# Optimization experiments

Hardware: AMD Instinct MI355X
Metric: run time of the kernel (lower is better)

Reference implementation:

```python
import math
import jax, jax.numpy as jnp
import numpy as np

D_MODEL = 1024
N_HEAD = 16
D_HEAD = 64
Q_LEN = 2048
MEM_LEN = 2048
K_LEN = MEM_LEN + Q_LEN
B = 1
LN_EPS = 1e-5


def setup_inputs() -> dict:
    key = jax.random.key(0)
    ks = jax.random.split(key, 8)
    hidden = jax.random.normal(ks[0], (B, Q_LEN, D_MODEL), dtype=jnp.float32)
    position_embedding = jax.random.normal(ks[1], (K_LEN, D_MODEL), dtype=jnp.float32)
    u = jax.random.normal(ks[2], (N_HEAD, D_HEAD), dtype=jnp.float32) * 0.02
    v = jax.random.normal(ks[3], (N_HEAD, D_HEAD), dtype=jnp.float32) * 0.02
    memory = jax.random.normal(ks[4], (B, MEM_LEN, D_MODEL), dtype=jnp.float32)
    # TXL causal mask: query i may attend to key j iff j <= i + MEM_LEN
    i = jnp.arange(Q_LEN)[:, None]
    j = jnp.arange(K_LEN)[None, :]
    mask = (j > (i + MEM_LEN))[None, None]  # (1,1,Q,K) bool, True = masked
    # weights (torch Linear has no bias here); stored as (in, out)
    s = 1.0 / math.sqrt(D_MODEL)
    W_qkv = jax.random.normal(ks[5], (D_MODEL, 3 * N_HEAD * D_HEAD), dtype=jnp.float32) * s
    W_pe = jax.random.normal(ks[6], (D_MODEL, N_HEAD * D_HEAD), dtype=jnp.float32) * s
    W_out = jax.random.normal(ks[7], (N_HEAD * D_HEAD, D_MODEL), dtype=jnp.float32) * (1.0 / math.sqrt(N_HEAD * D_HEAD))
    return {"hidden": hidden, "position_embedding": position_embedding, "u": u,
            "v": v, "mask": mask, "memory": memory,
            "W_qkv": W_qkv, "W_pe": W_pe, "W_out": W_out}


def _layer_norm(x):
    # elementwise_affine=False LayerNorm over last dim
    mu = jnp.mean(x, axis=-1, keepdims=True)
    var = jnp.var(x, axis=-1, keepdims=True)
    return (x - mu) / jnp.sqrt(var + LN_EPS)


def reference(hidden, position_embedding, u, v, mask, memory, W_qkv, W_pe, W_out):
    batch, q_len, _ = hidden.shape
    k_len = position_embedding.shape[0]
    scale = 1.0 / math.sqrt(D_HEAD)

    mh = jnp.concatenate([memory, hidden], axis=1)          # (B, k_len, d_model)
    qkv = mh @ W_qkv                                        # post-norm: no LN on input
    Q, K, V = jnp.split(qkv, 3, axis=-1)
    Q = Q[:, -q_len:, :]
    pe = position_embedding @ W_pe                          # (k_len, H*D)

    Q = Q.reshape(batch, q_len, N_HEAD, D_HEAD)
    K = K.reshape(batch, k_len, N_HEAD, D_HEAD)
    V = V.reshape(batch, k_len, N_HEAD, D_HEAD)
    pe = pe.reshape(batch, k_len, N_HEAD, D_HEAD)

    AC = jnp.einsum('bqhd,bkhd->bhqk', Q + u, K)
    BD = jnp.einsum('bqhd,bkhd->bhqk', Q + v, pe)
    # NOTE: the original module calls relative_shift(BD) but DISCARDS the
    # result, so BD is used unshifted. We faithfully reproduce that.
    score = (AC + BD) * scale
    score = jnp.where(mask, -jnp.inf, score)
    prob = jax.nn.softmax(score, axis=-1)                   # (B,H,Q,K)
    av = jnp.einsum('bhqk,bkhd->bqhd', prob, V)
    av = av.reshape(batch, q_len, N_HEAD * D_HEAD)
    attn_out = av @ W_out
    return _layer_norm(hidden + attn_out)                   # post-norm residual
```

## Files before the change

kernel.cpp:

```cpp
#include <hip/hip_runtime.h>

typedef __attribute__((ext_vector_type(4))) float f32x4;
typedef __attribute__((ext_vector_type(16))) float f32x16;
typedef __attribute__((ext_vector_type(8))) short bf16x8;
typedef __attribute__((ext_vector_type(4))) unsigned short u16x4;
typedef unsigned short u16;

#define DM 1024
#define NHEAD 16
#define DHEAD 64
#define QLEN 2048
#define MLEN 2048
#define KLEN 4096

__device__ __forceinline__ float bf2f(u16 u) {
    unsigned i = ((unsigned)u) << 16; float f; __builtin_memcpy(&f, &i, 4); return f;
}
__device__ __forceinline__ u16 f2bf(float f) {
    unsigned i; __builtin_memcpy(&i, &f, 4);
    unsigned r = i + 0x7fffu + ((i >> 16) & 1u);
    return (u16)(r >> 16);
}
__device__ __forceinline__ unsigned cvtpk_bf16(float lo, float hi) {
    unsigned r;
    asm("v_cvt_pk_bf16_f32 %0, %1, %2" : "=v"(r) : "v"(lo), "v"(hi));
    return r;
}
__device__ __forceinline__ void gl2lds16(const void* g, void* l) {
    __builtin_amdgcn_global_load_lds((const __attribute__((address_space(1))) void*)g,
                                     (__attribute__((address_space(3))) void*)l, 16, 0, 0);
}

__global__ __launch_bounds__(256) void prep(
    const float* __restrict__ memory, const float* __restrict__ hidden,
    const float* __restrict__ pos, const float* __restrict__ Wqkv,
    const float* __restrict__ Wpe, const float* __restrict__ Wout,
    u16* __restrict__ MH, u16* __restrict__ PEA,
    u16* __restrict__ WQKVT, u16* __restrict__ WPET, u16* __restrict__ WOUTT)
{
    __shared__ float ls[64][65];
    const int b = blockIdx.x, t = threadIdx.x;
    if (b < 8192) {
        size_t e = ((size_t)b * 256 + t) * 4;
        const size_t HALF = (size_t)KLEN * DM;
        f32x4 v; u16* dst;
        if (e < HALF) {
            size_t row = e >> 10, col = e & 1023;
            const float* src = (row < MLEN) ? (memory + row * DM) : (hidden + (row - MLEN) * DM);
            v = *(const f32x4*)(src + col);
            dst = MH + e;
        } else {
            size_t e2 = e - HALF;
            v = *(const f32x4*)(pos + e2);
            dst = PEA + e2;
        }
        u16x4 o;
        #pragma unroll
        for (int c = 0; c < 4; ++c) o[c] = f2bf(v[c]);
        *(u16x4*)dst = o;
        return;
    }
    int tb = b - 8192;
    const float* src; u16* dst; int N, bx, by;
    if (tb < 768)       { src = Wqkv; dst = WQKVT; N = 3 * DM; bx = tb % 48; by = tb / 48; }
    else if (tb < 1024) { int i = tb - 768;  src = Wpe;  dst = WPET;  N = DM; bx = i & 15; by = i >> 4; }
    else                { int i = tb - 1024; src = Wout; dst = WOUTT; N = DM; bx = i & 15; by = i >> 4; }
    const int n0 = bx * 64, k0 = by * 64;
    const int c = t & 63, rg = t >> 6;
    #pragma unroll
    for (int p = 0; p < 16; ++p) {
        int r = p * 4 + rg;
        ls[r][c] = src[(size_t)(k0 + r) * N + n0 + c];
    }
    __syncthreads();
    #pragma unroll
    for (int p = 0; p < 16; ++p) {
        int r = p * 4 + rg;
        dst[(size_t)(n0 + r) * DM + k0 + c] = f2bf(ls[c][r]);
    }
}

__global__ __launch_bounds__(256, 3) void gemm_qkvpe(
    const u16* __restrict__ MH, const u16* __restrict__ PEA,
    const u16* __restrict__ WQKVT, const u16* __restrict__ WPET,
    const float* __restrict__ u, const float* __restrict__ vv,
    u16* __restrict__ QHAT, u16* __restrict__ KHAT, u16* __restrict__ VB)
{
    __shared__ u16 lsA[128 * 64];
    __shared__ u16 lsB[128 * 64];
    const int b = blockIdx.x;
    int row0, col0, region; const u16 *A, *B;
    if (b < 512)      { row0 = (b >> 4) * 128; col0 = 1024 + (b & 15) * 128; A = MH; B = WQKVT;
                        region = (col0 < 2048) ? 1 : 2; }
    else if (b < 640) { int i = b - 512; row0 = 2048 + (i >> 3) * 128; col0 = (i & 7) * 128;
                        A = MH; B = WQKVT; region = 0; }
    else              { int i = b - 640; row0 = (i >> 3) * 128; col0 = (i & 7) * 128;
                        A = PEA; B = WPET; region = 3; }
    const int tid = threadIdx.x, wave = tid >> 6, lane = tid & 63;
    const int blk = lane >> 4, ln = lane & 15;
    const int wr = (wave >> 1) << 6, wc = (wave & 1) << 6;
    const int rstage = lane >> 3;
    const int cstage = (lane & 7) * 8;

    f32x4 acc[4][4];
    #pragma unroll
    for (int i = 0; i < 4; ++i)
        #pragma unroll
        for (int j = 0; j < 4; ++j) acc[i][j] = f32x4{0.f, 0.f, 0.f, 0.f};

    for (int k0 = 0; k0 < DM; k0 += 64) {
        #pragma unroll
        for (int t = 0; t < 4; ++t) {
            int chunk = wave * 4 + t;
            int r = chunk * 8 + rstage;
            gl2lds16(A + (size_t)(row0 + r) * DM + k0 + cstage, lsA + chunk * 512);
            gl2lds16(B + (size_t)(col0 + r) * DM + k0 + cstage, lsB + chunk * 512);
        }
        __syncthreads();
        #pragma unroll
        for (int kk = 0; kk < 2; ++kk) {
            bf16x8 af[4], bfr[4];
            #pragma unroll
            for (int i = 0; i < 4; ++i)
                af[i] = *(const bf16x8*)(lsA + (wr + i * 16 + ln) * 64 + kk * 32 + blk * 8);
            #pragma unroll
            for (int j = 0; j < 4; ++j)
                bfr[j] = *(const bf16x8*)(lsB + (wc + j * 16 + ln) * 64 + kk * 32 + blk * 8);
            #pragma unroll
            for (int i = 0; i < 4; ++i)
                #pragma unroll
                for (int j = 0; j < 4; ++j)
                    acc[i][j] = __builtin_amdgcn_mfma_f32_16x16x32_bf16(af[i], bfr[j], acc[i][j], 0, 0, 0);
        }
        __syncthreads();
    }
    #pragma unroll
    for (int i = 0; i < 4; ++i)
        #pragma unroll
        for (int j = 0; j < 4; ++j)
            #pragma unroll
            for (int r = 0; r < 4; ++r) {
                int row = row0 + wr + i * 16 + blk * 4 + r;
                int col = col0 + wc + j * 16 + ln;
                float val = acc[i][j][r];
                if (region == 0) {
                    int q = row - MLEN, h = col >> 6;
                    size_t base = ((size_t)h * QLEN + q) * 128 + (col & 63);
                    QHAT[base]      = f2bf((val + u[col]) * 0.125f);
                    QHAT[base + 64] = f2bf((val + vv[col]) * 0.125f);
                } else if (region == 1) {
                    int c = col - 1024, h = c >> 6;
                    KHAT[((size_t)h * KLEN + row) * 128 + (c & 63)] = f2bf(val);
                } else if (region == 2) {
                    VB[(size_t)row * DM + (col - 2048)] = f2bf(val);
                } else {
                    int h = col >> 6;
                    KHAT[((size_t)h * KLEN + row) * 128 + 64 + (col & 63)] = f2bf(val);
                }
            }
}

__global__ __launch_bounds__(256) void pack_vt(const u16* __restrict__ VB, u16* __restrict__ VT)
{
    __shared__ float ls[64][65];
    const int kt = blockIdx.x, h = blockIdx.y;
    const int t = threadIdx.x, c = t & 63, rg = t >> 6;
    #pragma unroll
    for (int p = 0; p < 16; ++p) {
        int r = p * 4 + rg;
        ls[r][c] = bf2f(VB[(size_t)(kt * 64 + r) * DM + h * 64 + c]);
    }
    __syncthreads();
    #pragma unroll
    for (int p = 0; p < 16; ++p) {
        int d = p * 4 + rg;
        VT[((size_t)h * DHEAD + d) * KLEN + kt * 64 + c] = f2bf(ls[c][d]);
    }
}

__global__ __launch_bounds__(256, 4) void attn_fused(
    const u16* __restrict__ QHAT, const u16* __restrict__ KHAT,
    const u16* __restrict__ VT, u16* __restrict__ OPb, float* __restrict__ ML)
{
    __shared__ __align__(16) u16 smem[18432];
    const int b = blockIdx.x;
    const int h  = ((b & 7) << 1) | ((b >> 3) & 1);
    const int ks = b >> 8;
    const int qb = (((b >> 4) & 15) + 4 * ks) & 15;
    const int tid = threadIdx.x;
    const int wave = tid >> 6, lane = tid & 63;
    const int l31 = lane & 31, hi = lane >> 5;
    const int qrow0 = qb * 128 + wave * 32;
    u16* pb = smem + 13312 + wave * 1280;
    const int px = (l31 >> 3) & 3;

    const u16* khp = KHAT + (size_t)h * KLEN * 128;
    const u16* vhp = VT + (size_t)h * DHEAD * KLEN;

    const int nt = qb + 17;
    const int kbase = ks * nt * 32;
    const int vd = tid >> 2, vc = tid & 3;
    const int vslot = vc ^ ((vd >> 3) & 3);

    auto stage_load = [&](int buf, int kt) -> bf16x8 {
        const int k0 = kbase + kt * 32;
        u16* Kb = smem + buf * 4096;
        #pragma unroll
        for (int i = 0; i < 2; ++i) {
            int c = i * 256 + tid;
            int row = c >> 4, cgl = c & 15;
            int cs = cgl ^ (row & 15);
            gl2lds16(khp + ((size_t)(k0 + row) << 7) + cs * 8,
                     Kb + (size_t)(i * 256 + (tid & ~63)) * 8);
        }
        return *(const bf16x8*)(vhp + (size_t)vd * KLEN + k0 + vc * 8);
    };
    auto stage_write = [&](int buf, bf16x8 vr) {
        *(bf16x8*)(smem + 8192 + buf * 2560 + vd * 40 + vslot * 8) = vr;
    };

    bf16x8 qf[8];
    {
        const u16* qbase = QHAT + ((size_t)h * QLEN + qrow0 + l31) * 128 + hi * 8;
        #pragma unroll
        for (int kd = 0; kd < 8; ++kd) qf[kd] = *(const bf16x8*)(qbase + kd * 16);
    }

    f32x16 oacc[2];
    #pragma unroll
    for (int dg = 0; dg < 2; ++dg)
        #pragma unroll
        for (int r = 0; r < 16; ++r) oacc[dg][r] = 0.f;
    float mi = -1e30f, li = 0.f;

    const int qlim = qrow0 + 31 + MLEN;
    const int qsel = qrow0 + l31 + MLEN;

    bf16x8 vreg = stage_load(0, 0);
    asm volatile("s_waitcnt vmcnt(0)" ::: "memory");
    stage_write(0, vreg);
    __syncthreads();

    int cur = 0;
    for (int kt = 0; kt < nt; ++kt) {
        const int k0 = kbase + kt * 32;
        const bool pre = (kt + 1 < nt);
        if (pre) vreg = stage_load(cur ^ 1, kt + 1);

        if (k0 <= qlim) {
            f32x16 sacc;
            #pragma unroll
            for (int r = 0; r < 16; ++r) sacc[r] = 0.f;
            const u16* kb = smem + cur * 4096;
            const int rx = l31 & 15;
            #pragma unroll
            for (int kd = 0; kd < 8; ++kd) {
                int cd = (kd * 2 + hi) ^ rx;
                bf16x8 kf = *(const bf16x8*)(kb + l31 * 128 + cd * 8);
                sacc = __builtin_amdgcn_mfma_f32_32x32x16_bf16(kf, qf[kd], sacc, 0, 0, 0);
            }
            if (k0 + 31 > qrow0 + MLEN) {
                const int keyb = k0 + 4 * hi;
                #pragma unroll
                for (int r = 0; r < 16; ++r) {
                    int key = keyb + (r & 3) + 8 * (r >> 2);
                    if (key > qsel) sacc[r] = -1e30f;
                }
            }
            float mt;
            {
                f32x4 m4;
                #pragma unroll
                for (int r = 0; r < 4; ++r)
                    m4[r] = fmaxf(fmaxf(sacc[r], sacc[4 + r]), fmaxf(sacc[8 + r], sacc[12 + r]));
                mt = fmaxf(fmaxf(m4[0], m4[1]), fmaxf(m4[2], m4[3]));
            }
            mt = fmaxf(mt, __shfl_xor(mt, 32, 64));
            if (!__all(mt <= mi)) {
                float mn = fmaxf(mi, mt);
                float corr = __expf(mi - mn);
                mi = mn;
                li *= corr;
                #pragma unroll
                for (int dg = 0; dg < 2; ++dg)
                    #pragma unroll
                    for (int r = 0; r < 16; ++r) oacc[dg][r] *= corr;
            }
            #pragma unroll
            for (int r = 0; r < 16; ++r) sacc[r] = __expf(sacc[r] - mi);
            float rs;
            {
                f32x4 s4;
                #pragma unroll
                for (int r = 0; r < 4; ++r)
                    s4[r] = (sacc[r] + sacc[4 + r]) + (sacc[8 + r] + sacc[12 + r]);
                rs = (s4[0] + s4[1]) + (s4[2] + s4[3]);
            }
            li += rs + __shfl_xor(rs, 32, 64);
            {
                unsigned* pd = (unsigned*)(pb + (size_t)l31 * 40);
                #pragma unroll
                for (int b2 = 0; b2 < 4; ++b2)
                    #pragma unroll
                    for (int c = 0; c < 2; ++c)
                        pd[(b2 ^ px) * 4 + 2 * hi + c] =
                            cvtpk_bf16(sacc[4 * b2 + 2 * c], sacc[4 * b2 + 2 * c + 1]);
            }
            #pragma unroll
            for (int kkl = 0; kkl < 2; ++kkl) {
                bf16x8 pf = *(const bf16x8*)(pb + (size_t)l31 * 40 + ((kkl * 2 + hi) ^ px) * 8);
                #pragma unroll
                for (int dg = 0; dg < 2; ++dg) {
                    int vrow = dg * 32 + l31;
                    int cd = (kkl * 2 + hi) ^ ((l31 >> 3) & 3);
                    bf16x8 vf = *(const bf16x8*)(smem + 8192 + cur * 2560 + vrow * 40 + cd * 8);
                    oacc[dg] = __builtin_amdgcn_mfma_f32_32x32x16_bf16(vf, pf, oacc[dg], 0, 0, 0);
                }
            }
        }
        asm volatile("s_waitcnt vmcnt(0)" ::: "memory");
        if (pre) stage_write(cur ^ 1, vreg);
        __syncthreads();
        cur ^= 1;
    }

    const int q = qrow0 + l31;
    unsigned* op32 = (unsigned*)(OPb + (((size_t)ks * QLEN + q) * NHEAD + h) * 64);
    #pragma unroll
    for (int dg = 0; dg < 2; ++dg) {
        union { f32x16 v; float f[16]; } oo;
        oo.v = oacc[dg];
        #pragma unroll
        for (int b2 = 0; b2 < 4; ++b2)
            #pragma unroll
            for (int c = 0; c < 2; ++c)
                op32[(dg * 32 + 8 * b2 + 4 * hi) / 2 + c] =
                    cvtpk_bf16(oo.f[4 * b2 + 2 * c], oo.f[4 * b2 + 2 * c + 1]);
    }
    if (!hi) {
        float* ml = ML + (((size_t)ks * QLEN + q) * NHEAD + h) * 2;
        ml[0] = mi; ml[1] = li;
    }
}

__global__ __launch_bounds__(256) void attn_combine(
    const u16* __restrict__ OPb, const float* __restrict__ ML, u16* __restrict__ AVB)
{
    int idx = blockIdx.x * 256 + threadIdx.x;
    int d8 = (idx & 7) * 8;
    int h  = (idx >> 3) & 15;
    int q  = idx >> 7;
    float m[4], l[4], mf = -1e30f;
    #pragma unroll
    for (int ks = 0; ks < 4; ++ks) {
        const float* ml = ML + (((size_t)ks * QLEN + q) * NHEAD + h) * 2;
        m[ks] = ml[0]; l[ks] = ml[1];
        mf = fmaxf(mf, m[ks]);
    }
    float lsum = 0.f;
    float a[4];
    #pragma unroll
    for (int ks = 0; ks < 4; ++ks) {
        a[ks] = __expf(m[ks] - mf);
        lsum += a[ks] * l[ks];
    }
    float inv = 1.f / lsum;
    float acc[8];
    #pragma unroll
    for (int j = 0; j < 8; ++j) acc[j] = 0.f;
    #pragma unroll
    for (int ks = 0; ks < 4; ++ks) {
        float w = a[ks] * inv;
        const u16* src = OPb + (((size_t)ks * QLEN + q) * NHEAD + h) * 64 + d8;
        u16x4 x0 = *(const u16x4*)(src);
        u16x4 x1 = *(const u16x4*)(src + 4);
        #pragma unroll
        for (int j = 0; j < 4; ++j) { acc[j] += w * bf2f(x0[j]); acc[4 + j] += w * bf2f(x1[j]); }
    }
    unsigned* A32 = (unsigned*)AVB;
    size_t base = ((size_t)q * DM + h * 64 + d8) >> 1;
    #pragma unroll
    for (int j = 0; j < 4; ++j)
        A32[base + j] = cvtpk_bf16(acc[2 * j], acc[2 * j + 1]);
}

__global__ __launch_bounds__(256, 3) void gemm_out(
    const u16* __restrict__ A, const u16* __restrict__ Bt, float* __restrict__ RES)
{
    __shared__ u16 lsA[128 * 64];
    __shared__ u16 lsB[128 * 64];
    const int b = blockIdx.x;
    const int tile = b >> 1, kh = b & 1;
    const int row0 = (tile >> 3) * 128, col0 = (tile & 7) * 128;
    const int tid = threadIdx.x, wave = tid >> 6, lane = tid & 63;
    const int blk = lane >> 4, ln = lane & 15;
    const int wr = (wave >> 1) << 6, wc = (wave & 1) << 6;
    const int rstage = lane >> 3;
    const int cstage = (lane & 7) * 8;

    f32x4 acc[4][4];
    #pragma unroll
    for (int i = 0; i < 4; ++i)
        #pragma unroll
        for (int j = 0; j < 4; ++j) acc[i][j] = f32x4{0.f, 0.f, 0.f, 0.f};

    for (int k0 = kh * 512; k0 < kh * 512 + 512; k0 += 64) {
        #pragma unroll
        for (int t = 0; t < 4; ++t) {
            int chunk = wave * 4 + t;
            int r = chunk * 8 + rstage;
            gl2lds16(A  + (size_t)(row0 + r) * DM + k0 + cstage, lsA + chunk * 512);
            gl2lds16(Bt + (size_t)(col0 + r) * DM + k0 + cstage, lsB + chunk * 512);
        }
        __syncthreads();
        #pragma unroll
        for (int kk = 0; kk < 2; ++kk) {
            bf16x8 af[4], bfr[4];
            #pragma unroll
            for (int i = 0; i < 4; ++i)
                af[i] = *(const bf16x8*)(lsA + (wr + i * 16 + ln) * 64 + kk * 32 + blk * 8);
            #pragma unroll
            for (int j = 0; j < 4; ++j)
                bfr[j] = *(const bf16x8*)(lsB + (wc + j * 16 + ln) * 64 + kk * 32 + blk * 8);
            #pragma unroll
            for (int i = 0; i < 4; ++i)
                #pragma unroll
                for (int j = 0; j < 4; ++j)
                    acc[i][j] = __builtin_amdgcn_mfma_f32_16x16x32_bf16(af[i], bfr[j], acc[i][j], 0, 0, 0);
        }
        __syncthreads();
    }
    float* C = RES + (size_t)kh * QLEN * DM;
    #pragma unroll
    for (int i = 0; i < 4; ++i)
        #pragma unroll
        for (int j = 0; j < 4; ++j)
            #pragma unroll
            for (int r = 0; r < 4; ++r) {
                int row = row0 + wr + i * 16 + blk * 4 + r;
                int col = col0 + wc + j * 16 + ln;
                C[(size_t)row * DM + col] = acc[i][j][r];
            }
}

__global__ __launch_bounds__(256) void ln_kernel(
    const float* __restrict__ hidden, const float* __restrict__ RES, float* __restrict__ out)
{
    const int row = blockIdx.x, t = threadIdx.x;
    const int wave = t >> 6, lane = t & 63;
    __shared__ float ws[8];
    f32x4 a = ((const f32x4*)(hidden + (size_t)row * DM))[t];
    f32x4 r0 = ((const f32x4*)(RES + (size_t)row * DM))[t];
    f32x4 r1 = ((const f32x4*)(RES + (size_t)(QLEN + row) * DM))[t];
    f32x4 v;
    #pragma unroll
    for (int c = 0; c < 4; ++c) v[c] = a[c] + r0[c] + r1[c];
    float s = v[0] + v[1] + v[2] + v[3];
    float s2 = v[0] * v[0] + v[1] * v[1] + v[2] * v[2] + v[3] * v[3];
    #pragma unroll
    for (int off = 1; off < 64; off <<= 1) {
        s += __shfl_xor(s, off, 64);
        s2 += __shfl_xor(s2, off, 64);
    }
    if (lane == 0) { ws[wave] = s; ws[4 + wave] = s2; }
    __syncthreads();
    float ts = ws[0] + ws[1] + ws[2] + ws[3];
    float ts2 = ws[4] + ws[5] + ws[6] + ws[7];
    float mu = ts * (1.f / DM);
    float var = ts2 * (1.f / DM) - mu * mu;
    float rsq = rsqrtf(var + 1e-5f);
    f32x4 o;
    #pragma unroll
    for (int c = 0; c < 4; ++c) o[c] = (v[c] - mu) * rsq;
    ((f32x4*)(out + (size_t)row * DM))[t] = o;
}

extern "C" void kernel_launch(void* const* d_in, const int* in_sizes, int n_in,
                              void* d_out, int out_size, void* d_ws, size_t ws_size,
                              hipStream_t stream)
{
    const float* hidden = (const float*)d_in[0];
    const float* pos    = (const float*)d_in[1];
    const float* u      = (const float*)d_in[2];
    const float* vv     = (const float*)d_in[3];
    const float* memory = (const float*)d_in[5];
    const float* Wqkv   = (const float*)d_in[6];
    const float* Wpe    = (const float*)d_in[7];
    const float* Wout   = (const float*)d_in[8];
    float* out = (float*)d_out;

    char* w = (char*)d_ws;
    auto alloc = [&](size_t bytes) {
        void* p = (void*)w;
        w += (bytes + 255) & ~(size_t)255;
        return p;
    };
    u16* MH    = (u16*)alloc((size_t)KLEN * DM * 2);
    u16* PEA   = (u16*)alloc((size_t)KLEN * DM * 2);
    u16* WQKVT = (u16*)alloc((size_t)3 * DM * DM * 2);
    u16* WPET  = (u16*)alloc((size_t)DM * DM * 2);
    u16* VB    = (u16*)alloc((size_t)KLEN * DM * 2);
    u16* QHAT  = (u16*)alloc((size_t)NHEAD * QLEN * 128 * 2);
    u16* KHAT  = (u16*)alloc((size_t)NHEAD * KLEN * 128 * 2);
    u16* VTb   = (u16*)alloc((size_t)NHEAD * DHEAD * KLEN * 2);
    u16* AVB   = (u16*)alloc((size_t)QLEN * DM * 2);
    float* RES = (float*)alloc((size_t)2 * QLEN * DM * 4);
    u16* WOUTT = (u16*)alloc((size_t)DM * DM * 2);
    u16* OPb   = (u16*)d_ws;
    float* ML  = (float*)((char*)d_ws + (size_t)4 * QLEN * NHEAD * 64 * 2);

    prep<<<8192 + 1280, 256, 0, stream>>>(memory, hidden, pos, Wqkv, Wpe, Wout,
                                          MH, PEA, WQKVT, WPET, WOUTT);
    gemm_qkvpe<<<896, 256, 0, stream>>>(MH, PEA, WQKVT, WPET, u, vv, QHAT, KHAT, VB);
    pack_vt<<<dim3(KLEN / 64, NHEAD), 256, 0, stream>>>(VB, VTb);
    attn_fused<<<dim3(1024), 256, 0, stream>>>(QHAT, KHAT, VTb, OPb, ML);
    attn_combine<<<dim3(QLEN * NHEAD * 8 / 256), 256, 0, stream>>>(OPb, ML, AVB);
    gemm_out<<<256, 256, 0, stream>>>(AVB, WOUTT, RES);
    ln_kernel<<<QLEN, 256, 0, stream>>>(hidden, RES, out);
}
```

Before: 163.4 us.

## Software-pipeline QK^T one tile ahead of softmax-PV and use exp2 with log2e-folded scale

The attention loop is restructured so the QK^T MFMA for the next key tile runs before the softmax and PV of the current tile. K and V loads are issued two tiles ahead using an unrolled A/B double buffer. The Q scale now folds in log2(e), so the exponentials become native exp2 instructions, and the combine kernel uses exp2 as well. Launch bounds drop from 4 to 3 waves per SIMD to give room for the extra live score registers, which may lower occupancy.

```diff
diff --git a/kernel.cpp b/kernel.cpp
--- a/kernel.cpp
+++ b/kernel.cpp
@@ -12,6 +12,7 @@
 #define QLEN 2048
 #define MLEN 2048
 #define KLEN 4096
+#define QSCALE 0.18033688011112042f
 
 __device__ __forceinline__ float bf2f(u16 u) {
     unsigned i = ((unsigned)u) << 16; float f; __builtin_memcpy(&f, &i, 4); return f;
@@ -20,6 +21,13 @@
     unsigned i; __builtin_memcpy(&i, &f, 4);
     unsigned r = i + 0x7fffu + ((i >> 16) & 1u);
     return (u16)(r >> 16);
+}
+__device__ __forceinline__ float exp2_fast(float x) {
+#if __has_builtin(__builtin_amdgcn_exp2f)
+    return __builtin_amdgcn_exp2f(x);
+#else
+    return exp2f(x);
+#endif
 }
 __device__ __forceinline__ unsigned cvtpk_bf16(float lo, float hi) {
     unsigned r;
@@ -146,8 +154,8 @@
                 if (region == 0) {
                     int q = row - MLEN, h = col >> 6;
                     size_t base = ((size_t)h * QLEN + q) * 128 + (col & 63);
-                    QHAT[base]      = f2bf((val + u[col]) * 0.125f);
-                    QHAT[base + 64] = f2bf((val + vv[col]) * 0.125f);
+                    QHAT[base]      = f2bf((val + u[col]) * QSCALE);
+                    QHAT[base + 64] = f2bf((val + vv[col]) * QSCALE);
                 } else if (region == 1) {
                     int c = col - 1024, h = c >> 6;
                     KHAT[((size_t)h * KLEN + row) * 128 + (c & 63)] = f2bf(val);
@@ -178,7 +186,7 @@
     }
 }
 
-__global__ __launch_bounds__(256, 4) void attn_fused(
+__global__ __launch_bounds__(256, 3) void attn_fused(
     const u16* __restrict__ QHAT, const u16* __restrict__ KHAT,
     const u16* __restrict__ VT, u16* __restrict__ OPb, float* __restrict__ ML)
 {
@@ -202,7 +210,10 @@
     const int vd = tid >> 2, vc = tid & 3;
     const int vslot = vc ^ ((vd >> 3) & 3);
 
-    auto stage_load = [&](int buf, int kt) -> bf16x8 {
+    const int qlim = qrow0 + 31 + MLEN;
+    const int qsel = qrow0 + l31 + MLEN;
+
+    auto stageK = [&](int buf, int kt) {
         const int k0 = kbase + kt * 32;
         u16* Kb = smem + buf * 4096;
         #pragma unroll
@@ -213,9 +224,11 @@
             gl2lds16(khp + ((size_t)(k0 + row) << 7) + cs * 8,
                      Kb + (size_t)(i * 256 + (tid & ~63)) * 8);
         }
-        return *(const bf16x8*)(vhp + (size_t)vd * KLEN + k0 + vc * 8);
     };
-    auto stage_write = [&](int buf, bf16x8 vr) {
+    auto loadV = [&](int kt) -> bf16x8 {
+        return *(const bf16x8*)(vhp + (size_t)vd * KLEN + kbase + kt * 32 + vc * 8);
+    };
+    auto writeV = [&](int buf, bf16x8 vr) {
         *(bf16x8*)(smem + 8192 + buf * 2560 + vd * 40 + vslot * 8) = vr;
     };
 
@@ -233,95 +246,112 @@
         for (int r = 0; r < 16; ++r) oacc[dg][r] = 0.f;
     float mi = -1e30f, li = 0.f;
 
-    const int qlim = qrow0 + 31 + MLEN;
-    const int qsel = qrow0 + l31 + MLEN;
-
-    bf16x8 vreg = stage_load(0, 0);
+    auto qk = [&](int buf) -> f32x16 {
+        f32x16 s;
+        #pragma unroll
+        for (int r = 0; r < 16; ++r) s[r] = 0.f;
+        const u16* kb = smem + buf * 4096;
+        const int rx = l31 & 15;
+        #pragma unroll
+        for (int kd = 0; kd < 8; ++kd) {
+            int cd = (kd * 2 + hi) ^ rx;
+            bf16x8 kf = *(const bf16x8*)(kb + l31 * 128 + cd * 8);
+            s = __builtin_amdgcn_mfma_f32_32x32x16_bf16(kf, qf[kd], s, 0, 0, 0);
+        }
+        return s;
+    };
+
+    auto smpv = [&](f32x16& sacc, int buf, int k0) {
+        if (k0 + 31 > qrow0 + MLEN) {
+            const int keyb = k0 + 4 * hi;
+            #pragma unroll
+            for (int r = 0; r < 16; ++r) {
+                int key = keyb + (r & 3) + 8 * (r >> 2);
+                if (key > qsel) sacc[r] = -1e30f;
+            }
+        }
+        float mt;
+        {
+            f32x4 m4;
+            #pragma unroll
+            for (int r = 0; r < 4; ++r)
+                m4[r] = fmaxf(fmaxf(sacc[r], sacc[4 + r]), fmaxf(sacc[8 + r], sacc[12 + r]));
+            mt = fmaxf(fmaxf(m4[0], m4[1]), fmaxf(m4[2], m4[3]));
+        }
+        mt = fmaxf(mt, __shfl_xor(mt, 32, 64));
+        if (!__all(mt <= mi)) {
+            float mn = fmaxf(mi, mt);
+            float corr = exp2_fast(mi - mn);
+            mi = mn;
+            li *= corr;
+            #pragma unroll
+            for (int dg = 0; dg < 2; ++dg)
+                #pragma unroll
+                for (int r = 0; r < 16; ++r) oacc[dg][r] *= corr;
+        }
+        #pragma unroll
+        for (int r = 0; r < 16; ++r) sacc[r] = exp2_fast(sacc[r] - mi);
+        float rs;
+        {
+            f32x4 s4;
+            #pragma unroll
+            for (int r = 0; r < 4; ++r)
+                s4[r] = (sacc[r] + sacc[4 + r]) + (sacc[8 + r] + sacc[12 + r]);
+            rs = (s4[0] + s4[1]) + (s4[2] + s4[3]);
+        }
+        li += rs + __shfl_xor(rs, 32, 64);
+        {
+            unsigned* pd = (unsigned*)(pb + (size_t)l31 * 40);
+            #pragma unroll
+            for (int b2 = 0; b2 < 4; ++b2)
+                #pragma unroll
+                for (int c = 0; c < 2; ++c)
+                    pd[(b2 ^ px) * 4 + 2 * hi + c] =
+                        cvtpk_bf16(sacc[4 * b2 + 2 * c], sacc[4 * b2 + 2 * c + 1]);
+        }
+        #pragma unroll
+        for (int kkl = 0; kkl < 2; ++kkl) {
+            bf16x8 pf = *(const bf16x8*)(pb + (size_t)l31 * 40 + ((kkl * 2 + hi) ^ px) * 8);
+            #pragma unroll
+            for (int dg = 0; dg < 2; ++dg) {
+                int vrow = dg * 32 + l31;
+                int cd = (kkl * 2 + hi) ^ ((l31 >> 3) & 3);
+                bf16x8 vf = *(const bf16x8*)(smem + 8192 + buf * 2560 + vrow * 40 + cd * 8);
+                oacc[dg] = __builtin_amdgcn_mfma_f32_32x32x16_bf16(vf, pf, oacc[dg], 0, 0, 0);
+            }
+        }
+    };
+
+    stageK(0, 0);
+    bf16x8 vrA = loadV(0);
+    bf16x8 vrB = vrA;
+    if (nt > 1) { stageK(1, 1); vrB = loadV(1); }
     asm volatile("s_waitcnt vmcnt(0)" ::: "memory");
-    stage_write(0, vreg);
     __syncthreads();
-
-    int cur = 0;
-    for (int kt = 0; kt < nt; ++kt) {
-        const int k0 = kbase + kt * 32;
-        const bool pre = (kt + 1 < nt);
-        if (pre) vreg = stage_load(cur ^ 1, kt + 1);
-
-        if (k0 <= qlim) {
-            f32x16 sacc;
-            #pragma unroll
-            for (int r = 0; r < 16; ++r) sacc[r] = 0.f;
-            const u16* kb = smem + cur * 4096;
-            const int rx = l31 & 15;
-            #pragma unroll
-            for (int kd = 0; kd < 8; ++kd) {
-                int cd = (kd * 2 + hi) ^ rx;
-                bf16x8 kf = *(const bf16x8*)(kb + l31 * 128 + cd * 8);
-                sacc = __builtin_amdgcn_mfma_f32_32x32x16_bf16(kf, qf[kd], sacc, 0, 0, 0);
-            }
-            if (k0 + 31 > qrow0 + MLEN) {
-                const int keyb = k0 + 4 * hi;
-                #pragma unroll
-                for (int r = 0; r < 16; ++r) {
-                    int key = keyb + (r & 3) + 8 * (r >> 2);
-                    if (key > qsel) sacc[r] = -1e30f;
-                }
-            }
-            float mt;
-            {
-                f32x4 m4;
-                #pragma unroll
-                for (int r = 0; r < 4; ++r)
-                    m4[r] = fmaxf(fmaxf(sacc[r], sacc[4 + r]), fmaxf(sacc[8 + r], sacc[12 + r]));
-                mt = fmaxf(fmaxf(m4[0], m4[1]), fmaxf(m4[2], m4[3]));
-            }
-            mt = fmaxf(mt, __shfl_xor(mt, 32, 64));
-            if (!__all(mt <= mi)) {
-                float mn = fmaxf(mi, mt);
-                float corr = __expf(mi - mn);
-                mi = mn;
-                li *= corr;
-                #pragma unroll
-                for (int dg = 0; dg < 2; ++dg)
-                    #pragma unroll
-                    for (int r = 0; r < 16; ++r) oacc[dg][r] *= corr;
-            }
-            #pragma unroll
-            for (int r = 0; r < 16; ++r) sacc[r] = __expf(sacc[r] - mi);
-            float rs;
-            {
-                f32x4 s4;
-                #pragma unroll
-                for (int r = 0; r < 4; ++r)
-                    s4[r] = (sacc[r] + sacc[4 + r]) + (sacc[8 + r] + sacc[12 + r]);
-                rs = (s4[0] + s4[1]) + (s4[2] + s4[3]);
-            }
-            li += rs + __shfl_xor(rs, 32, 64);
-            {
-                unsigned* pd = (unsigned*)(pb + (size_t)l31 * 40);
-                #pragma unroll
-                for (int b2 = 0; b2 < 4; ++b2)
-                    #pragma unroll
-                    for (int c = 0; c < 2; ++c)
-                        pd[(b2 ^ px) * 4 + 2 * hi + c] =
-                            cvtpk_bf16(sacc[4 * b2 + 2 * c], sacc[4 * b2 + 2 * c + 1]);
-            }
-            #pragma unroll
-            for (int kkl = 0; kkl < 2; ++kkl) {
-                bf16x8 pf = *(const bf16x8*)(pb + (size_t)l31 * 40 + ((kkl * 2 + hi) ^ px) * 8);
-                #pragma unroll
-                for (int dg = 0; dg < 2; ++dg) {
-                    int vrow = dg * 32 + l31;
-                    int cd = (kkl * 2 + hi) ^ ((l31 >> 3) & 3);
-                    bf16x8 vf = *(const bf16x8*)(smem + 8192 + cur * 2560 + vrow * 40 + cd * 8);
-                    oacc[dg] = __builtin_amdgcn_mfma_f32_32x32x16_bf16(vf, pf, oacc[dg], 0, 0, 0);
-                }
-            }
-        }
-        asm volatile("s_waitcnt vmcnt(0)" ::: "memory");
-        if (pre) stage_write(cur ^ 1, vreg);
-        __syncthreads();
-        cur ^= 1;
+    f32x16 sA = qk(0);
+    writeV(0, vrA);
+    __syncthreads();
+    f32x16 sB;
+
+    for (int t = 0; t < nt; t += 2) {
+        {
+            const int k0 = kbase + t * 32;
+            if (t + 2 < nt) { stageK(0, t + 2); vrA = loadV(t + 2); }
+            if (t + 1 < nt) sB = qk(1);
+            if (k0 <= qlim) smpv(sA, 0, k0);
+            if (t + 1 < nt) writeV(1, vrB);
+            asm volatile("s_waitcnt vmcnt(0)" ::: "memory");
+            __syncthreads();
+        }
+        if (t + 1 < nt) {
+            const int k0 = kbase + (t + 1) * 32;
+            if (t + 3 < nt) { stageK(1, t + 3); vrB = loadV(t + 3); }
+            if (t + 2 < nt) sA = qk(0);
+            if (k0 <= qlim) smpv(sB, 1, k0);
+            if (t + 2 < nt) writeV(0, vrA);
+            asm volatile("s_waitcnt vmcnt(0)" ::: "memory");
+            __syncthreads();
+        }
     }
 
     const int q = qrow0 + l31;
@@ -361,7 +391,7 @@
     float a[4];
     #pragma unroll
     for (int ks = 0; ks < 4; ++ks) {
-        a[ks] = __expf(m[ks] - mf);
+        a[ks] = exp2_fast(m[ks] - mf);
         lsum += a[ks] * l[ks];
     }
     float inv = 1.f / lsum;
```

Measured after the change: 175.5 us. +7.4%, slower.
